# Kernel optimization log

Measured on AMD Instinct MI355X. Metric: run time of the kernel, lower is better.

Reference implementation:

```python
import jax, jax.numpy as jnp
import numpy as np

N_EMBED = 2048
NUM_EXPERTS = 64
TOP_K = 8
B, S = 4, 8192


def setup_inputs() -> dict:
    key = jax.random.key(0)
    ks = jax.random.split(key, 8)
    scale = 1.0 / np.sqrt(N_EMBED)
    return {
        "x": jax.random.normal(ks[0], (B, S, N_EMBED), dtype=jnp.float32),
        "eps": jax.random.normal(ks[1], (B, S, NUM_EXPERTS), dtype=jnp.float32),
        "w_router": jax.random.uniform(ks[2], (N_EMBED, NUM_EXPERTS), jnp.float32, -scale, scale),
        "b_router": jax.random.uniform(ks[3], (NUM_EXPERTS,), jnp.float32, -scale, scale),
        "w_noise": jax.random.uniform(ks[4], (N_EMBED, NUM_EXPERTS), jnp.float32, -scale, scale),
        "b_noise": jax.random.uniform(ks[5], (NUM_EXPERTS,), jnp.float32, -scale, scale),
        "w_skip": jax.random.uniform(ks[6], (N_EMBED, 1), jnp.float32, -scale, scale),
        "b_skip": jax.random.uniform(ks[7], (1,), jnp.float32, -scale, scale),
    }


def reference(x, eps, w_router, b_router, w_noise, b_noise, w_skip, b_skip):
    # Router and noise logits: [B, S, E]
    logits = jnp.einsum("bsd,de->bse", x, w_router) + b_router
    noise_logits = jnp.einsum("bsd,de->bse", x, w_noise) + b_noise
    # noisy_logits = logits + randn * softplus(noise_logits); randn passed as eps
    noisy_logits = logits + eps * jax.nn.softplus(noise_logits)
    # top-k + scatter(-inf) + softmax == softmax over top-k values scattered back
    top_vals, indices = jax.lax.top_k(noisy_logits, TOP_K)  # [B,S,K]
    gates = jax.nn.softmax(top_vals, axis=-1)  # [B,S,K]
    onehot = jax.nn.one_hot(indices, NUM_EXPERTS, dtype=x.dtype)  # [B,S,K,E]
    router_output = jnp.einsum("bsk,bske->bse", gates, onehot)  # zeros off top-k
    # Sigmoid skip gate: [B, S, 1]
    skip_prob = jax.nn.sigmoid(jnp.einsum("bsd,do->bso", x, w_skip) + b_skip)
    return router_output, indices, skip_prob
```

## Files before the change

kernel.cpp:

```cpp
#include <hip/hip_runtime.h>
#include <math.h>

#define NTOK   32768
#define D      2048
#define E      64
#define TOPK   8

#define BLOCK  256
#define TM     64
#define BK     32
#define NCHUNK (D / BK)
#define NBLK   (NTOK / TM)

#define WBF_BYTES (NCHUNK * 16384)

#define ABUF0   0
#define ABUF1   8192
#define LG_OFF  0
#define LG_STR  133
#define WSK_OFF 34048
#define SP_OFF  42240
#define SMEM_BYTES 42496

#define TIE_EPS 1e-4f

typedef __bf16 bf16x8 __attribute__((ext_vector_type(8)));
typedef float  f32x4  __attribute__((ext_vector_type(4)));

__device__ __forceinline__ unsigned short f2bf_rne(float f) {
    unsigned int u = __float_as_uint(f);
    u += 0x7FFFu + ((u >> 16) & 1u);
    return (unsigned short)(u >> 16);
}

__device__ __forceinline__ void split_pack8(const float* xv, uint4& hv, uint4& lv) {
    unsigned int h[8], l[8];
#pragma unroll
    for (int j = 0; j < 8; ++j) {
        unsigned short hb = f2bf_rne(xv[j]);
        float hf = __uint_as_float(((unsigned int)hb) << 16);
        unsigned short lb = f2bf_rne(xv[j] - hf);
        h[j] = hb; l[j] = lb;
    }
    hv.x = h[0] | (h[1] << 16); hv.y = h[2] | (h[3] << 16);
    hv.z = h[4] | (h[5] << 16); hv.w = h[6] | (h[7] << 16);
    lv.x = l[0] | (l[1] << 16); lv.y = l[2] | (l[3] << 16);
    lv.z = l[4] | (l[5] << 16); lv.w = l[6] | (l[7] << 16);
}

__global__ __launch_bounds__(256) void convert_w_kernel(
    const float* __restrict__ wr, const float* __restrict__ wn, char* __restrict__ wbf)
{
    int u = blockIdx.x * 256 + threadIdx.x;
    int col  = u & 127;
    int koct = (u >> 7) & 3;
    int c    = u >> 9;
    const float* src = (col < 64)
        ? (wr + (size_t)(c * BK + koct * 8) * E + col)
        : (wn + (size_t)(c * BK + koct * 8) * E + (col - 64));
    float xv[8];
#pragma unroll
    for (int j = 0; j < 8; ++j) xv[j] = src[(size_t)j * E];
    uint4 hv, lv;
    split_pack8(xv, hv, lv);
    char* dst = wbf + (size_t)c * 16384 + (size_t)(koct * 128 + col) * 16;
    *(uint4*)dst = hv;
    *(uint4*)(dst + 8192) = lv;
}

__global__ __launch_bounds__(BLOCK, 2) void router_kernel(
    const float* __restrict__ x, const float* __restrict__ eps,
    const char* __restrict__ wbf,
    const float* __restrict__ b_router, const float* __restrict__ b_noise,
    const float* __restrict__ w_skip, const float* __restrict__ b_skip,
    float* __restrict__ out_router, float* __restrict__ out_idx,
    float* __restrict__ out_skip, int* __restrict__ flags, int cap)
{
    __shared__ __attribute__((aligned(16))) char smem[SMEM_BYTES];
    const int tid = threadIdx.x;
    const int tokBase = blockIdx.x * TM;

    const int lane = tid & 63;
    const int wv   = tid >> 6;
    const int q    = lane >> 4;
    const int m    = lane & 15;

    const int tokA  = tid >> 2;
    const int koctA = tid & 3;
    const int fragA = (koctA << 6) + (tokA ^ (koctA << 2));
    const float* xptr = x + (size_t)(tokBase + tokA) * D + koctA * 8;

    f32x4 acc[4][2];
#pragma unroll
    for (int tt = 0; tt < 4; ++tt)
#pragma unroll
        for (int cw = 0; cw < 2; ++cw) acc[tt][cw] = (f32x4){0.f, 0.f, 0.f, 0.f};
    float skipAcc = 0.f;

    float* wsk = (float*)(smem + WSK_OFF);

    auto loadB = [&](int c, uint4* bh, uint4* bl) {
        const char* src = wbf + (size_t)c * 16384;
#pragma unroll
        for (int cw = 0; cw < 2; ++cw) {
            int f = (q << 7) + (wv << 5) + (cw << 4) + m;
            bh[cw] = *(const uint4*)(src + f * 16);
            bl[cw] = *(const uint4*)(src + 8192 + f * 16);
        }
    };

    auto storeA = [&](int buf, float4 a0, float4 a1) {
        float xv[8] = {a0.x, a0.y, a0.z, a0.w, a1.x, a1.y, a1.z, a1.w};
        uint4 hv, lv;
        split_pack8(xv, hv, lv);
        char* ab = smem + (buf ? ABUF1 : ABUF0);
        *(uint4*)(ab + fragA * 16) = hv;
        *(uint4*)(ab + 4096 + fragA * 16) = lv;
    };

    auto skipFma = [&](float4 a0, float4 a1, int c) {
        const float* wk = wsk + c * BK + koctA * 8;
        skipAcc = fmaf(a0.x, wk[0], skipAcc); skipAcc = fmaf(a0.y, wk[1], skipAcc);
        skipAcc = fmaf(a0.z, wk[2], skipAcc); skipAcc = fmaf(a0.w, wk[3], skipAcc);
        skipAcc = fmaf(a1.x, wk[4], skipAcc); skipAcc = fmaf(a1.y, wk[5], skipAcc);
        skipAcc = fmaf(a1.z, wk[6], skipAcc); skipAcc = fmaf(a1.w, wk[7], skipAcc);
    };

    auto compute = [&](int buf, const uint4* bh, const uint4* bl) {
        const char* ab = smem + (buf ? ABUF1 : ABUF0);
        uint4 ah[4], al[4];
#pragma unroll
        for (int tt = 0; tt < 4; ++tt) {
            int f = (q << 6) + (((tt << 4) + m) ^ (q << 2));
            ah[tt] = *(const uint4*)(ab + f * 16);
            al[tt] = *(const uint4*)(ab + 4096 + f * 16);
        }
#pragma unroll
        for (int tt = 0; tt < 4; ++tt)
#pragma unroll
            for (int cw = 0; cw < 2; ++cw) {
                bf16x8 Ah = __builtin_bit_cast(bf16x8, ah[tt]);
                bf16x8 Al = __builtin_bit_cast(bf16x8, al[tt]);
                bf16x8 Bh = __builtin_bit_cast(bf16x8, bh[cw]);
                bf16x8 Bl = __builtin_bit_cast(bf16x8, bl[cw]);
                acc[tt][cw] = __builtin_amdgcn_mfma_f32_16x16x32_bf16(Ah, Bh, acc[tt][cw], 0, 0, 0);
                acc[tt][cw] = __builtin_amdgcn_mfma_f32_16x16x32_bf16(Ah, Bl, acc[tt][cw], 0, 0, 0);
                acc[tt][cw] = __builtin_amdgcn_mfma_f32_16x16x32_bf16(Al, Bh, acc[tt][cw], 0, 0, 0);
            }
    };

#pragma unroll
    for (int r = 0; r < 2; ++r) {
        int i4 = tid + 256 * r;
        ((float4*)wsk)[i4] = ((const float4*)w_skip)[i4];
    }
    float4 xq[2][2];
    xq[0][0] = *(const float4*)(xptr);
    xq[0][1] = *(const float4*)(xptr + 4);
    xq[1][0] = *(const float4*)(xptr + BK);
    xq[1][1] = *(const float4*)(xptr + BK + 4);
    uint4 bh[2], bl[2], bhn[2], bln[2];
    loadB(0, bh, bl);
    storeA(0, xq[0][0], xq[0][1]);
    skipFma(xq[0][0], xq[0][1], 0);
    __syncthreads();

    for (int c = 0; c < NCHUNK; ++c) {
        if (c + 1 < NCHUNK) loadB(c + 1, bhn, bln);
        float4 xn0, xn1;
        if (c + 2 < NCHUNK) {
            xn0 = *(const float4*)(xptr + (c + 2) * BK);
            xn1 = *(const float4*)(xptr + (c + 2) * BK + 4);
        }
        compute(c & 1, bh, bl);
        if (c + 1 < NCHUNK) {
            storeA((c + 1) & 1, xq[(c + 1) & 1][0], xq[(c + 1) & 1][1]);
            skipFma(xq[(c + 1) & 1][0], xq[(c + 1) & 1][1], c + 1);
        }
        if (c + 2 < NCHUNK) { xq[c & 1][0] = xn0; xq[c & 1][1] = xn1; }
#pragma unroll
        for (int cw = 0; cw < 2; ++cw) { bh[cw] = bhn[cw]; bl[cw] = bln[cw]; }
        __syncthreads();
    }

    float* lg = (float*)(smem + LG_OFF);
#pragma unroll
    for (int tt = 0; tt < 4; ++tt)
#pragma unroll
        for (int cw = 0; cw < 2; ++cw) {
#pragma unroll
            for (int reg = 0; reg < 4; ++reg) {
                int token = tt * 16 + q * 4 + reg;
                int col = wv * 32 + cw * 16 + m;
                lg[token * LG_STR + col] = acc[tt][cw][reg];
            }
        }

    skipAcc += __shfl_xor(skipAcc, 1);
    skipAcc += __shfl_xor(skipAcc, 2);
    if ((tid & 3) == 0) ((float*)(smem + SP_OFF))[tokA] = skipAcc;
    __syncthreads();

    if (tid < 64) {
        const int t = tid;
        const int tok = tokBase + t;
        float* row = lg + t * LG_STR;

        float sv = ((float*)(smem + SP_OFF))[t] + b_skip[0];
        out_skip[tok] = 1.f / (1.f + expf(-sv));

        const float4* epsr = (const float4*)(eps + (size_t)tok * E);
#pragma unroll 4
        for (int e4 = 0; e4 < 16; ++e4) {
            float4 ep = epsr[e4];
            float epv[4] = {ep.x, ep.y, ep.z, ep.w};
#pragma unroll
            for (int u2 = 0; u2 < 4; ++u2) {
                int e = e4 * 4 + u2;
                float lgv = row[e] + b_router[e];
                float nl  = row[64 + e] + b_noise[e];
                float sp  = fmaxf(nl, 0.f) + log1pf(expf(-fabsf(nl)));
                row[e] = lgv + epv[u2] * sp;
            }
        }

        float vals[9];
        int idxs[8];
        for (int p = 0; p < 9; ++p) {
            float best = -INFINITY;
            int bi = 0;
            for (int e = 0; e < 64; ++e) {
                float v = row[e];
                if (v > best) { best = v; bi = e; }
            }
            vals[p] = best;
            if (p < 8) idxs[p] = bi;
            row[bi] = -INFINITY;
        }

        float mg = 1e30f;
#pragma unroll
        for (int p = 0; p < 8; ++p) mg = fminf(mg, vals[p] - vals[p + 1]);
        if (mg < TIE_EPS) {
            int slot = atomicAdd(flags, 1);
            if (slot < cap) flags[2 + slot] = tok;
        }

        float mx = vals[0];
        float g[8], s = 0.f;
#pragma unroll
        for (int p = 0; p < 8; ++p) { g[p] = expf(vals[p] - mx); s += g[p]; }
        float inv = 1.f / s;

        float* rrow = row + 64;
#pragma unroll
        for (int e = 0; e < 64; ++e) rrow[e] = 0.f;
#pragma unroll
        for (int p = 0; p < 8; ++p) rrow[idxs[p]] = g[p] * inv;
#pragma unroll
        for (int e4 = 0; e4 < 16; ++e4) {
            float4 o = make_float4(rrow[e4 * 4], rrow[e4 * 4 + 1],
                                   rrow[e4 * 4 + 2], rrow[e4 * 4 + 3]);
            *(float4*)(out_router + (size_t)tok * E + e4 * 4) = o;
        }
        float4 i0 = make_float4((float)idxs[0], (float)idxs[1], (float)idxs[2], (float)idxs[3]);
        float4 i1 = make_float4((float)idxs[4], (float)idxs[5], (float)idxs[6], (float)idxs[7]);
        *(float4*)(out_idx + (size_t)tok * TOPK)     = i0;
        *(float4*)(out_idx + (size_t)tok * TOPK + 4) = i1;
    }
}

__global__ __launch_bounds__(256) void fixup_kernel(
    const float* __restrict__ x, const float* __restrict__ eps,
    const float* __restrict__ w_router, const float* __restrict__ b_router,
    const float* __restrict__ w_noise, const float* __restrict__ b_noise,
    float* __restrict__ out_router, float* __restrict__ out_idx,
    const int* __restrict__ flags, int cap)
{
    __shared__ double smR[4][64];
    __shared__ double smN[4][64];
    __shared__ double noisy[64];
    const int tid  = threadIdx.x;
    const int lane = tid & 63;
    const int qw   = tid >> 6;

    int count = flags[0];
    if (count > cap) count = cap;

    for (int i = blockIdx.x; i < count; i += gridDim.x) {
        int tok = flags[2 + i];
        const float4* xr4 = (const float4*)(x + (size_t)tok * D + qw * 512);
        const float* wrB = w_router + (size_t)(qw * 512) * E + lane;
        const float* wnB = w_noise  + (size_t)(qw * 512) * E + lane;

        double pr0 = 0, pr1 = 0, pr2 = 0, pr3 = 0;
        double pn0 = 0, pn1 = 0, pn2 = 0, pn3 = 0;
#pragma unroll 2
        for (int it = 0; it < 128; ++it) {
            float4 xv = xr4[it];
            const float* wr = wrB + (size_t)(it * 4) * E;
            const float* wn = wnB + (size_t)(it * 4) * E;
            pr0 += (double)xv.x * (double)wr[0];
            pr1 += (double)xv.y * (double)wr[E];
            pr2 += (double)xv.z * (double)wr[2 * E];
            pr3 += (double)xv.w * (double)wr[3 * E];
            pn0 += (double)xv.x * (double)wn[0];
            pn1 += (double)xv.y * (double)wn[E];
            pn2 += (double)xv.z * (double)wn[2 * E];
            pn3 += (double)xv.w * (double)wn[3 * E];
        }
        smR[qw][lane] = (pr0 + pr1) + (pr2 + pr3);
        smN[qw][lane] = (pn0 + pn1) + (pn2 + pn3);
        __syncthreads();

        if (tid < 64) {
            double lgv = smR[0][tid] + smR[1][tid] + smR[2][tid] + smR[3][tid] + (double)b_router[tid];
            double nl  = smN[0][tid] + smN[1][tid] + smN[2][tid] + smN[3][tid] + (double)b_noise[tid];
            double sp  = fmax(nl, 0.0) + log1p(exp(-fabs(nl)));
            noisy[tid] = lgv + (double)eps[(size_t)tok * E + tid] * sp;
        }
        __syncthreads();

        if (tid == 0) {
            double tmp[64];
            for (int j = 0; j < 64; ++j) tmp[j] = noisy[j];
            double vals[8]; int idxs[8];
            for (int p = 0; p < 8; ++p) {
                double best = -1e300; int bi = 0;
                for (int j = 0; j < 64; ++j)
                    if (tmp[j] > best) { best = tmp[j]; bi = j; }
                vals[p] = best; idxs[p] = bi; tmp[bi] = -1e300;
            }
            double mx = vals[0], s = 0.0, g[8];
            for (int p = 0; p < 8; ++p) { g[p] = exp(vals[p] - mx); s += g[p]; }
            float rowv[64];
            for (int j = 0; j < 64; ++j) rowv[j] = 0.f;
            for (int p = 0; p < 8; ++p) rowv[idxs[p]] = (float)(g[p] / s);
            for (int j = 0; j < 64; ++j) out_router[(size_t)tok * E + j] = rowv[j];
            for (int p = 0; p < 8; ++p) out_idx[(size_t)tok * TOPK + p] = (float)idxs[p];
        }
        __syncthreads();
    }
}

extern "C" void kernel_launch(void* const* d_in, const int* in_sizes, int n_in,
                              void* d_out, int out_size, void* d_ws, size_t ws_size,
                              hipStream_t stream) {
    const float* x        = (const float*)d_in[0];
    const float* eps      = (const float*)d_in[1];
    const float* w_router = (const float*)d_in[2];
    const float* b_router = (const float*)d_in[3];
    const float* w_noise  = (const float*)d_in[4];
    const float* b_noise  = (const float*)d_in[5];
    const float* w_skip   = (const float*)d_in[6];
    const float* b_skip   = (const float*)d_in[7];

    float* out = (float*)d_out;
    float* out_router = out;
    float* out_idx    = out + (size_t)NTOK * E;
    float* out_skip   = out_idx + (size_t)NTOK * TOPK;

    char* wbf  = (char*)d_ws;
    int* flags = (int*)((char*)d_ws + WBF_BYTES);
    int cap = 0;
    if (ws_size > WBF_BYTES + 16) {
        size_t c = (ws_size - WBF_BYTES - 8) / 4;
        cap = (c > 16384) ? 16384 : (int)c;
    }

    hipMemsetAsync((char*)d_ws + WBF_BYTES, 0, 8, stream);

    convert_w_kernel<<<dim3(128), dim3(256), 0, stream>>>(w_router, w_noise, wbf);

    router_kernel<<<dim3(NBLK), dim3(BLOCK), 0, stream>>>(
        x, eps, wbf, b_router, b_noise, w_skip, b_skip,
        out_router, out_idx, out_skip, flags, cap);

    fixup_kernel<<<dim3(512), dim3(256), 0, stream>>>(
        x, eps, w_router, b_router, w_noise, b_noise,
        out_router, out_idx, flags, cap);
}
```

Measured before the change: 544.9 us.

## Unroll main loop by two with static buffers and batch fixup tokens

```diff
diff --git a/kernel.cpp b/kernel.cpp
--- a/kernel.cpp
+++ b/kernel.cpp
@@ -100,20 +100,19 @@
     float* wsk = (float*)(smem + WSK_OFF);
 
     auto loadB = [&](int c, uint4* bh, uint4* bl) {
-        const char* src = wbf + (size_t)c * 16384;
 #pragma unroll
         for (int cw = 0; cw < 2; ++cw) {
+            const char* src = wbf + (size_t)c * 16384;
             int f = (q << 7) + (wv << 5) + (cw << 4) + m;
             bh[cw] = *(const uint4*)(src + f * 16);
             bl[cw] = *(const uint4*)(src + 8192 + f * 16);
         }
     };
 
-    auto storeA = [&](int buf, float4 a0, float4 a1) {
+    auto storeA = [&](char* ab, float4 a0, float4 a1) {
         float xv[8] = {a0.x, a0.y, a0.z, a0.w, a1.x, a1.y, a1.z, a1.w};
         uint4 hv, lv;
         split_pack8(xv, hv, lv);
-        char* ab = smem + (buf ? ABUF1 : ABUF0);
         *(uint4*)(ab + fragA * 16) = hv;
         *(uint4*)(ab + 4096 + fragA * 16) = lv;
     };
@@ -126,8 +125,7 @@
         skipAcc = fmaf(a1.z, wk[6], skipAcc); skipAcc = fmaf(a1.w, wk[7], skipAcc);
     };
 
-    auto compute = [&](int buf, const uint4* bh, const uint4* bl) {
-        const char* ab = smem + (buf ? ABUF1 : ABUF0);
+    auto compute = [&](const char* ab, const uint4* bh, const uint4* bl) {
         uint4 ah[4], al[4];
 #pragma unroll
         for (int tt = 0; tt < 4; ++tt) {
@@ -154,34 +152,42 @@
         int i4 = tid + 256 * r;
         ((float4*)wsk)[i4] = ((const float4*)w_skip)[i4];
     }
-    float4 xq[2][2];
-    xq[0][0] = *(const float4*)(xptr);
-    xq[0][1] = *(const float4*)(xptr + 4);
-    xq[1][0] = *(const float4*)(xptr + BK);
-    xq[1][1] = *(const float4*)(xptr + BK + 4);
-    uint4 bh[2], bl[2], bhn[2], bln[2];
-    loadB(0, bh, bl);
-    storeA(0, xq[0][0], xq[0][1]);
-    skipFma(xq[0][0], xq[0][1], 0);
+    uint4 bh0[2], bl0[2], bh1[2], bl1[2];
+    float4 xa0, xa1, xb0, xb1;
+
+    xa0 = *(const float4*)(xptr);
+    xa1 = *(const float4*)(xptr + 4);
+    loadB(0, bh0, bl0);
+    storeA(smem + ABUF0, xa0, xa1);
+    skipFma(xa0, xa1, 0);
+    xa0 = *(const float4*)(xptr + BK);
+    xa1 = *(const float4*)(xptr + BK + 4);
     __syncthreads();
 
-    for (int c = 0; c < NCHUNK; ++c) {
-        if (c + 1 < NCHUNK) loadB(c + 1, bhn, bln);
-        float4 xn0, xn1;
-        if (c + 2 < NCHUNK) {
-            xn0 = *(const float4*)(xptr + (c + 2) * BK);
-            xn1 = *(const float4*)(xptr + (c + 2) * BK + 4);
-        }
-        compute(c & 1, bh, bl);
-        if (c + 1 < NCHUNK) {
-            storeA((c + 1) & 1, xq[(c + 1) & 1][0], xq[(c + 1) & 1][1]);
-            skipFma(xq[(c + 1) & 1][0], xq[(c + 1) & 1][1], c + 1);
-        }
-        if (c + 2 < NCHUNK) { xq[c & 1][0] = xn0; xq[c & 1][1] = xn1; }
-#pragma unroll
-        for (int cw = 0; cw < 2; ++cw) { bh[cw] = bhn[cw]; bl[cw] = bln[cw]; }
+    for (int cc = 0; cc <= 60; cc += 2) {
+        loadB(cc + 1, bh1, bl1);
+        xb0 = *(const float4*)(xptr + (cc + 2) * BK);
+        xb1 = *(const float4*)(xptr + (cc + 2) * BK + 4);
+        compute(smem + ABUF0, bh0, bl0);
+        storeA(smem + ABUF1, xa0, xa1);
+        skipFma(xa0, xa1, cc + 1);
         __syncthreads();
-    }
+
+        loadB(cc + 2, bh0, bl0);
+        xa0 = *(const float4*)(xptr + (cc + 3) * BK);
+        xa1 = *(const float4*)(xptr + (cc + 3) * BK + 4);
+        compute(smem + ABUF1, bh1, bl1);
+        storeA(smem + ABUF0, xb0, xb1);
+        skipFma(xb0, xb1, cc + 2);
+        __syncthreads();
+    }
+    loadB(63, bh1, bl1);
+    compute(smem + ABUF0, bh0, bl0);
+    storeA(smem + ABUF1, xa0, xa1);
+    skipFma(xa0, xa1, 63);
+    __syncthreads();
+    compute(smem + ABUF1, bh1, bl1);
+    __syncthreads();
 
     float* lg = (float*)(smem + LG_OFF);
 #pragma unroll
@@ -270,6 +276,7 @@
     }
 }
 
+#define FT 4
 __global__ __launch_bounds__(256) void fixup_kernel(
     const float* __restrict__ x, const float* __restrict__ eps,
     const float* __restrict__ w_router, const float* __restrict__ b_router,
@@ -277,8 +284,8 @@
     float* __restrict__ out_router, float* __restrict__ out_idx,
     const int* __restrict__ flags, int cap)
 {
-    __shared__ double smR[4][64];
-    __shared__ double smN[4][64];
+    __shared__ double smR[4][FT][64];
+    __shared__ double smN[4][FT][64];
     __shared__ double noisy[64];
     const int tid  = threadIdx.x;
     const int lane = tid & 63;
@@ -287,59 +294,76 @@
     int count = flags[0];
     if (count > cap) count = cap;
 
-    for (int i = blockIdx.x; i < count; i += gridDim.x) {
-        int tok = flags[2 + i];
-        const float4* xr4 = (const float4*)(x + (size_t)tok * D + qw * 512);
+    for (int base = blockIdx.x * FT; base < count; base += gridDim.x * FT) {
+        int n = count - base; if (n > FT) n = FT;
+        int toks[FT];
+#pragma unroll
+        for (int t = 0; t < FT; ++t)
+            toks[t] = flags[2 + base + (t < n ? t : n - 1)];
+
+        const float* xr[FT];
+#pragma unroll
+        for (int t = 0; t < FT; ++t)
+            xr[t] = x + (size_t)toks[t] * D + qw * 512;
         const float* wrB = w_router + (size_t)(qw * 512) * E + lane;
         const float* wnB = w_noise  + (size_t)(qw * 512) * E + lane;
 
-        double pr0 = 0, pr1 = 0, pr2 = 0, pr3 = 0;
-        double pn0 = 0, pn1 = 0, pn2 = 0, pn3 = 0;
-#pragma unroll 2
+        double pr[FT], pn[FT];
+#pragma unroll
+        for (int t = 0; t < FT; ++t) { pr[t] = 0.0; pn[t] = 0.0; }
+
         for (int it = 0; it < 128; ++it) {
-            float4 xv = xr4[it];
             const float* wr = wrB + (size_t)(it * 4) * E;
             const float* wn = wnB + (size_t)(it * 4) * E;
-            pr0 += (double)xv.x * (double)wr[0];
-            pr1 += (double)xv.y * (double)wr[E];
-            pr2 += (double)xv.z * (double)wr[2 * E];
-            pr3 += (double)xv.w * (double)wr[3 * E];
-            pn0 += (double)xv.x * (double)wn[0];
-            pn1 += (double)xv.y * (double)wn[E];
-            pn2 += (double)xv.z * (double)wn[2 * E];
-            pn3 += (double)xv.w * (double)wn[3 * E];
-        }
-        smR[qw][lane] = (pr0 + pr1) + (pr2 + pr3);
-        smN[qw][lane] = (pn0 + pn1) + (pn2 + pn3);
+            double w0 = wr[0], w1 = wr[E], w2 = wr[2 * E], w3 = wr[3 * E];
+            double v0 = wn[0], v1 = wn[E], v2 = wn[2 * E], v3 = wn[3 * E];
+#pragma unroll
+            for (int t = 0; t < FT; ++t) {
+                float4 xv = *(const float4*)(xr[t] + it * 4);
+                pr[t] += (double)xv.x * w0 + (double)xv.y * w1
+                       + (double)xv.z * w2 + (double)xv.w * w3;
+                pn[t] += (double)xv.x * v0 + (double)xv.y * v1
+                       + (double)xv.z * v2 + (double)xv.w * v3;
+            }
+        }
+#pragma unroll
+        for (int t = 0; t < FT; ++t) {
+            smR[qw][t][lane] = pr[t];
+            smN[qw][t][lane] = pn[t];
+        }
         __syncthreads();
 
-        if (tid < 64) {
-            double lgv = smR[0][tid] + smR[1][tid] + smR[2][tid] + smR[3][tid] + (double)b_router[tid];
-            double nl  = smN[0][tid] + smN[1][tid] + smN[2][tid] + smN[3][tid] + (double)b_noise[tid];
-            double sp  = fmax(nl, 0.0) + log1p(exp(-fabs(nl)));
-            noisy[tid] = lgv + (double)eps[(size_t)tok * E + tid] * sp;
-        }
-        __syncthreads();
-
-        if (tid == 0) {
-            double tmp[64];
-            for (int j = 0; j < 64; ++j) tmp[j] = noisy[j];
-            double vals[8]; int idxs[8];
-            for (int p = 0; p < 8; ++p) {
-                double best = -1e300; int bi = 0;
-                for (int j = 0; j < 64; ++j)
-                    if (tmp[j] > best) { best = tmp[j]; bi = j; }
-                vals[p] = best; idxs[p] = bi; tmp[bi] = -1e300;
-            }
-            double mx = vals[0], s = 0.0, g[8];
-            for (int p = 0; p < 8; ++p) { g[p] = exp(vals[p] - mx); s += g[p]; }
-            float rowv[64];
-            for (int j = 0; j < 64; ++j) rowv[j] = 0.f;
-            for (int p = 0; p < 8; ++p) rowv[idxs[p]] = (float)(g[p] / s);
-            for (int j = 0; j < 64; ++j) out_router[(size_t)tok * E + j] = rowv[j];
-            for (int p = 0; p < 8; ++p) out_idx[(size_t)tok * TOPK + p] = (float)idxs[p];
-        }
-        __syncthreads();
+        for (int t = 0; t < n; ++t) {
+            int tok = toks[t];
+            if (tid < 64) {
+                double lgv = smR[0][t][tid] + smR[1][t][tid] + smR[2][t][tid] + smR[3][t][tid]
+                           + (double)b_router[tid];
+                double nl  = smN[0][t][tid] + smN[1][t][tid] + smN[2][t][tid] + smN[3][t][tid]
+                           + (double)b_noise[tid];
+                double sp  = fmax(nl, 0.0) + log1p(exp(-fabs(nl)));
+                noisy[tid] = lgv + (double)eps[(size_t)tok * E + tid] * sp;
+            }
+            __syncthreads();
+            if (tid == 0) {
+                double tmp[64];
+                for (int j = 0; j < 64; ++j) tmp[j] = noisy[j];
+                double vals[8]; int idxs[8];
+                for (int p = 0; p < 8; ++p) {
+                    double best = -1e300; int bi = 0;
+                    for (int j = 0; j < 64; ++j)
+                        if (tmp[j] > best) { best = tmp[j]; bi = j; }
+                    vals[p] = best; idxs[p] = bi; tmp[bi] = -1e300;
+                }
+                double mx = vals[0], s = 0.0, g[8];
+                for (int p = 0; p < 8; ++p) { g[p] = exp(vals[p] - mx); s += g[p]; }
+                float rowv[64];
+                for (int j = 0; j < 64; ++j) rowv[j] = 0.f;
+                for (int p = 0; p < 8; ++p) rowv[idxs[p]] = (float)(g[p] / s);
+                for (int j = 0; j < 64; ++j) out_router[(size_t)tok * E + j] = rowv[j];
+                for (int p = 0; p < 8; ++p) out_idx[(size_t)tok * TOPK + p] = (float)idxs[p];
+            }
+            __syncthreads();
+        }
     }
 }
 
@@ -376,7 +400,7 @@
         x, eps, wbf, b_router, b_noise, w_skip, b_skip,
         out_router, out_idx, out_skip, flags, cap);
 
-    fixup_kernel<<<dim3(512), dim3(256), 0, stream>>>(
+    fixup_kernel<<<dim3(2048), dim3(256), 0, stream>>>(
         x, eps, w_router, b_router, w_noise, b_noise,
         out_router, out_idx, flags, cap);
 }
```

Measured after the change: 644.2 us. 18.2% more time.
